# Optimization experiments

Hardware: AMD Instinct MI355X
Metric: run time of the kernel (lower is better)

Reference implementation:

```python
import jax, jax.numpy as jnp
import numpy as np


def setup_inputs() -> dict:
    key = jax.random.key(0)
    k1, k2, k3 = jax.random.split(key, 3)
    B, T, S, D = 8, 2048, 2048, 512
    main_input = jax.random.normal(k1, (B, T, D), dtype=jnp.float32)
    attn_input = jax.random.normal(k2, (B, S, D), dtype=jnp.float32)
    # f_input is a torch Linear(D, D): y = x @ W_f.T + b_f
    W_f = jax.random.normal(k3, (D, D), dtype=jnp.float32) * (1.0 / np.sqrt(D))
    b_f = jnp.zeros((D,), dtype=jnp.float32)
    return {"main_input": main_input, "attn_input": attn_input, "W_f": W_f, "b_f": b_f}


def reference(main_input, attn_input, W_f, b_f):
    # keys: f_input applied to each attn word  [B,S,D]
    keys = jnp.einsum("bsd,ed->bse", attn_input, W_f) + b_f
    # scores[b,t,s] = keys[b,s,:] . main_input[b,t,:]
    scores = jnp.einsum("bse,bte->bts", keys, main_input)
    attn = jax.nn.softmax(scores, axis=-1)  # softmax over attn words S
    # weighted sum of RAW attn_input (values are unprojected)
    out = jnp.einsum("bts,bsd->btd", attn, attn_input)
    return out
```

## Files before the change

### kernel.cpp

```cpp
#include <hip/hip_runtime.h>
#include <math.h>

#define B_  8
#define T_  2048
#define S_  2048
#define D_  512

typedef _Float16 half8   __attribute__((ext_vector_type(8)));
typedef _Float16 half4_t __attribute__((ext_vector_type(4)));
typedef float    floatx4 __attribute__((ext_vector_type(4)));

__device__ __forceinline__ floatx4 mfma16(half8 a, half8 b, floatx4 c) {
  return __builtin_amdgcn_mfma_f32_16x16x32_f16(a, b, c, 0, 0, 0);
}

__device__ __forceinline__ void async16(void* lds, const void* g) {
  __builtin_amdgcn_global_load_lds(
      (const __attribute__((address_space(1))) void*)g,
      (__attribute__((address_space(3))) void*)lds, 16, 0, 0);
}

__global__ __launch_bounds__(256) void transpose_cast_kernel(
    const float* __restrict__ attn, _Float16* __restrict__ Vt) {
  __shared__ _Float16 tile[32][33];
  const int tx = threadIdx.x, ty = threadIdx.y;
  const int b = blockIdx.z, s0 = blockIdx.y * 32, d0 = blockIdx.x * 32;
  const float* src = attn + ((size_t)b * S_ + s0) * D_ + d0;
#pragma unroll
  for (int i = 0; i < 4; ++i) {
    int s = ty + i * 8;
    tile[tx][s] = (_Float16)src[(size_t)s * D_ + tx];
  }
  __syncthreads();
  _Float16* dst = Vt + ((size_t)b * D_ + d0) * S_ + s0;
#pragma unroll
  for (int i = 0; i < 4; ++i) {
    int d = ty + i * 8;
    dst[(size_t)d * S_ + tx] = tile[d][tx];
  }
}

__global__ __launch_bounds__(512, 2) void keys_gemm_kernel(
    const float* __restrict__ X, const float* __restrict__ W,
    const float* __restrict__ bias, _Float16* __restrict__ K16) {
  __shared__ alignas(16) _Float16 Xs[128][72];
  __shared__ alignas(16) _Float16 Ws[128][72];
  const int t = threadIdx.x;
  const int wave = t >> 6, lane = t & 63, q = lane >> 4, n = lane & 15;
  const int wm = wave >> 2, wn = wave & 3;
  const int m0 = blockIdx.x * 128, n0 = blockIdx.y * 128;

  floatx4 acc[4][2];
#pragma unroll
  for (int i = 0; i < 4; ++i)
#pragma unroll
    for (int j = 0; j < 2; ++j) {
      floatx4 z = {0.f, 0.f, 0.f, 0.f};
      acc[i][j] = z;
    }

  for (int kc = 0; kc < 8; ++kc) {
    const int k0 = kc * 64;
#pragma unroll
    for (int i = 0; i < 4; ++i) {
      int seg = i * 512 + t;
      int row = seg >> 4, c4 = (seg & 15) * 4;
      floatx4 xv = *(const floatx4*)&X[(size_t)(m0 + row) * D_ + k0 + c4];
      floatx4 wv = *(const floatx4*)&W[(size_t)(n0 + row) * D_ + k0 + c4];
      half4_t xh, wh;
#pragma unroll
      for (int j = 0; j < 4; ++j) { xh[j] = (_Float16)xv[j]; wh[j] = (_Float16)wv[j]; }
      *(half4_t*)&Xs[row][c4] = xh;
      *(half4_t*)&Ws[row][c4] = wh;
    }
    __syncthreads();
#pragma unroll
    for (int kk = 0; kk < 2; ++kk) {
      half8 a[4], bb[2];
#pragma unroll
      for (int mt = 0; mt < 4; ++mt)
        a[mt] = *(const half8*)&Xs[wm * 64 + mt * 16 + n][kk * 32 + q * 8];
#pragma unroll
      for (int nt = 0; nt < 2; ++nt)
        bb[nt] = *(const half8*)&Ws[wn * 32 + nt * 16 + n][kk * 32 + q * 8];
#pragma unroll
      for (int mt = 0; mt < 4; ++mt)
#pragma unroll
        for (int nt = 0; nt < 2; ++nt)
          acc[mt][nt] = mfma16(a[mt], bb[nt], acc[mt][nt]);
    }
    __syncthreads();
  }

#pragma unroll
  for (int nt = 0; nt < 2; ++nt) {
    int col = n0 + wn * 32 + nt * 16 + n;
    float bv = bias[col];
#pragma unroll
    for (int mt = 0; mt < 4; ++mt)
#pragma unroll
      for (int r = 0; r < 4; ++r) {
        int row = m0 + wm * 64 + mt * 16 + q * 4 + r;
        K16[(size_t)row * D_ + col] = (_Float16)(acc[mt][nt][r] + bv);
      }
  }
}

__global__ __launch_bounds__(256, 1) void flash_kernel(
    const float* __restrict__ Qf, const _Float16* __restrict__ K16,
    const _Float16* __restrict__ Vt, float* __restrict__ out) {
  __shared__ _Float16 Klds[2][32][512];
  __shared__ _Float16 Vlds[2][512][32];
  __shared__ _Float16 Pscr[4][16][40];

  const int t = threadIdx.x;
  const int w = t >> 6, lane = t & 63, qd = lane >> 4, n = lane & 15;
  const int n7 = n & 7;
  const int bid = blockIdx.x;
  const int b = bid & 7, t0 = (bid >> 3) * 64;

  const _Float16* Kb = K16 + (size_t)b * S_ * D_;
  const _Float16* Vb = Vt + (size_t)b * D_ * S_;

  const int ksw = lane ^ 0;
  const int vsw = (lane & 3) ^ ((lane >> 3) & 3);
  const int ccV = qd ^ ((n >> 1) & 3);

  half8 qreg[16];
  {
    const float* qrow = Qf + ((size_t)b * T_ + t0 + w * 16 + n) * D_;
#pragma unroll
    for (int kk = 0; kk < 16; ++kk) {
      floatx4 v0 = *(const floatx4*)&qrow[kk * 32 + qd * 8];
      floatx4 v1 = *(const floatx4*)&qrow[kk * 32 + qd * 8 + 4];
      half8 h;
#pragma unroll
      for (int j = 0; j < 4; ++j) { h[j] = (_Float16)v0[j]; h[j + 4] = (_Float16)v1[j]; }
      qreg[kk] = h;
    }
  }

  floatx4 O[33];
#pragma unroll
  for (int ng = 0; ng < 33; ++ng) {
    floatx4 z = {0.f, 0.f, 0.f, 0.f};
    O[ng] = z;
  }
  float m_st[4];
#pragma unroll
  for (int r = 0; r < 4; ++r) m_st[r] = -1e30f;

  half8 ones8;
#pragma unroll
  for (int j = 0; j < 8; ++j) ones8[j] = (_Float16)1.0f;

#pragma unroll
  for (int i = 0; i < 8; ++i) {
    int row = w * 8 + i;
    async16(&Klds[0][row][0], Kb + (size_t)row * D_ + ((lane ^ (row & 7)) * 8));
  }
#pragma unroll
  for (int i = 0; i < 8; ++i) {
    int d0 = (w * 8 + i) * 16;
    async16(&Vlds[0][d0][0], Vb + (size_t)(d0 + (lane >> 2)) * S_ + vsw * 8);
  }
  __syncthreads();

  for (int st = 0; st < S_ / 32; ++st) {
    const int cur = st & 1, nxt = cur ^ 1;
    const int s0 = st * 32;

    if (st < S_ / 32 - 1) {
#pragma unroll
      for (int i = 0; i < 8; ++i) {
        int row = w * 8 + i;
        async16(&Klds[nxt][row][0],
                Kb + (size_t)(s0 + 32 + row) * D_ + ((lane ^ (row & 7)) * 8));
      }
#pragma unroll
      for (int i = 0; i < 8; ++i) {
        int d0 = (w * 8 + i) * 16;
        async16(&Vlds[nxt][d0][0],
                Vb + (size_t)(d0 + (lane >> 2)) * S_ + s0 + 32 + vsw * 8);
      }
    }

    floatx4 Sa0 = {0.f, 0.f, 0.f, 0.f}, Sa1 = Sa0, Sb0 = Sa0, Sb1 = Sa0;
#pragma unroll
    for (int kk = 0; kk < 8; ++kk) {
      int slot = (kk * 4 + qd) ^ n7;
      half8 b0 = *(const half8*)&Klds[cur][n][slot * 8];
      half8 b1 = *(const half8*)&Klds[cur][16 + n][slot * 8];
      Sa0 = mfma16(qreg[kk], b0, Sa0);
      Sa1 = mfma16(qreg[kk], b1, Sa1);
    }
#pragma unroll
    for (int kk = 8; kk < 16; ++kk) {
      int slot = (kk * 4 + qd) ^ n7;
      half8 b0 = *(const half8*)&Klds[cur][n][slot * 8];
      half8 b1 = *(const half8*)&Klds[cur][16 + n][slot * 8];
      Sb0 = mfma16(qreg[kk], b0, Sb0);
      Sb1 = mfma16(qreg[kk], b1, Sb1);
    }
    floatx4 Sc0 = Sa0 + Sb0, Sc1 = Sa1 + Sb1;

    float alpha[4];
#pragma unroll
    for (int r = 0; r < 4; ++r) {
      float v = fmaxf(Sc0[r], Sc1[r]);
      v = fmaxf(v, __shfl_xor(v, 1, 16));
      v = fmaxf(v, __shfl_xor(v, 2, 16));
      v = fmaxf(v, __shfl_xor(v, 4, 16));
      v = fmaxf(v, __shfl_xor(v, 8, 16));
      float mn = fmaxf(m_st[r], v);
      alpha[r] = __expf(m_st[r] - mn);
      m_st[r] = mn;
    }

    bool unchanged = (alpha[0] == 1.f) & (alpha[1] == 1.f) &
                     (alpha[2] == 1.f) & (alpha[3] == 1.f);
    if (!__all(unchanged)) {
#pragma unroll
      for (int ng = 0; ng < 33; ++ng)
#pragma unroll
        for (int r = 0; r < 4; ++r) O[ng][r] *= alpha[r];
    }

#pragma unroll
    for (int r = 0; r < 4; ++r) {
      float p0 = __expf(Sc0[r] - m_st[r]);
      float p1 = __expf(Sc1[r] - m_st[r]);
      Pscr[w][qd * 4 + r][n] = (_Float16)p0;
      Pscr[w][qd * 4 + r][16 + n] = (_Float16)p1;
    }
    half8 av = *(const half8*)&Pscr[w][n][qd * 8];

#pragma unroll
    for (int ng = 0; ng < 32; ++ng) {
      half8 bv = *(const half8*)&Vlds[cur][ng * 16 + n][ccV * 8];
      O[ng] = mfma16(av, bv, O[ng]);
    }
    O[32] = mfma16(av, ones8, O[32]);

    if (st < S_ / 32 - 1) __syncthreads();
  }

  float* ob = out + ((size_t)b * T_ + t0 + w * 16) * D_;
#pragma unroll
  for (int r = 0; r < 4; ++r) {
    float inv = 1.f / O[32][r];
    const size_t rowoff = (size_t)(qd * 4 + r) * D_;
#pragma unroll
    for (int ng = 0; ng < 32; ++ng)
      ob[rowoff + ng * 16 + n] = O[ng][r] * inv;
  }
}

extern "C" void kernel_launch(void* const* d_in, const int* in_sizes, int n_in,
                              void* d_out, int out_size, void* d_ws, size_t ws_size,
                              hipStream_t stream) {
  (void)in_sizes; (void)n_in; (void)out_size; (void)ws_size;
  const float* main_in = (const float*)d_in[0];
  const float* attn_in = (const float*)d_in[1];
  const float* W_f     = (const float*)d_in[2];
  const float* b_f     = (const float*)d_in[3];
  float* out = (float*)d_out;

  _Float16* K16 = (_Float16*)d_ws;
  _Float16* Vt  = K16 + (size_t)B_ * S_ * D_;

  transpose_cast_kernel<<<dim3(D_ / 32, S_ / 32, B_), dim3(32, 8, 1), 0, stream>>>(
      attn_in, Vt);
  keys_gemm_kernel<<<dim3((B_ * S_) / 128, D_ / 128), 512, 0, stream>>>(
      attn_in, W_f, b_f, K16);
  flash_kernel<<<(B_ * T_) / 64, 256, 0, stream>>>(main_in, K16, Vt, out);
}
```

Measured before the change: 314.2 us.

## Split flash output dim across 8 waves and prestage fp16 inputs for keys GEMM

The flash kernel now runs 8 waves per block. Two waves share each 16-row query group and each computes half of the 512-wide output, which halves the O accumulator registers and targets two blocks per CU. The Q·K score computation is now done twice, once by each of the two waves in a pair. The keys GEMM now reads fp16 copies of X (written by the transpose kernel) and W (written by a new cast kernel) through async global-to-LDS loads with double buffering and 4x4 MFMA tiles per wave. This adds an extra fp16 workspace write plus one more kernel launch, and the V LDS swizzle was removed, which may cause bank conflicts.

```diff
diff --git a/kernel.cpp b/kernel.cpp
--- a/kernel.cpp
+++ b/kernel.cpp
@@ -21,7 +21,8 @@
 }
 
 __global__ __launch_bounds__(256) void transpose_cast_kernel(
-    const float* __restrict__ attn, _Float16* __restrict__ Vt) {
+    const float* __restrict__ attn, _Float16* __restrict__ Vt,
+    _Float16* __restrict__ X16) {
   __shared__ _Float16 tile[32][33];
   const int tx = threadIdx.x, ty = threadIdx.y;
   const int b = blockIdx.z, s0 = blockIdx.y * 32, d0 = blockIdx.x * 32;
@@ -29,7 +30,9 @@
 #pragma unroll
   for (int i = 0; i < 4; ++i) {
     int s = ty + i * 8;
-    tile[tx][s] = (_Float16)src[(size_t)s * D_ + tx];
+    _Float16 h = (_Float16)src[(size_t)s * D_ + tx];
+    tile[tx][s] = h;
+    X16[((size_t)b * S_ + s0 + s) * D_ + d0 + tx] = h;
   }
   __syncthreads();
   _Float16* dst = Vt + ((size_t)b * D_ + d0) * S_ + s0;
@@ -40,95 +43,105 @@
   }
 }
 
-__global__ __launch_bounds__(512, 2) void keys_gemm_kernel(
-    const float* __restrict__ X, const float* __restrict__ W,
+__global__ __launch_bounds__(256) void wcast_kernel(
+    const float* __restrict__ W, _Float16* __restrict__ W16) {
+  int idx = (blockIdx.x * 256 + threadIdx.x) * 4;
+  floatx4 v = *(const floatx4*)&W[idx];
+  half4_t h;
+#pragma unroll
+  for (int j = 0; j < 4; ++j) h[j] = (_Float16)v[j];
+  *(half4_t*)&W16[idx] = h;
+}
+
+__global__ __launch_bounds__(256, 2) void keys_gemm_kernel(
+    const _Float16* __restrict__ X16, const _Float16* __restrict__ W16,
     const float* __restrict__ bias, _Float16* __restrict__ K16) {
-  __shared__ alignas(16) _Float16 Xs[128][72];
-  __shared__ alignas(16) _Float16 Ws[128][72];
+  __shared__ _Float16 As[2][128 * 32];
+  __shared__ _Float16 Bs[2][128 * 32];
   const int t = threadIdx.x;
-  const int wave = t >> 6, lane = t & 63, q = lane >> 4, n = lane & 15;
-  const int wm = wave >> 2, wn = wave & 3;
+  const int w = t >> 6, lane = t & 63, qd = lane >> 4, n = lane & 15;
+  const int wm = w >> 1, wn = w & 1;
   const int m0 = blockIdx.x * 128, n0 = blockIdx.y * 128;
 
-  floatx4 acc[4][2];
+  floatx4 acc[4][4];
 #pragma unroll
   for (int i = 0; i < 4; ++i)
 #pragma unroll
-    for (int j = 0; j < 2; ++j) {
+    for (int j = 0; j < 4; ++j) {
       floatx4 z = {0.f, 0.f, 0.f, 0.f};
       acc[i][j] = z;
     }
 
-  for (int kc = 0; kc < 8; ++kc) {
-    const int k0 = kc * 64;
-#pragma unroll
-    for (int i = 0; i < 4; ++i) {
-      int seg = i * 512 + t;
-      int row = seg >> 4, c4 = (seg & 15) * 4;
-      floatx4 xv = *(const floatx4*)&X[(size_t)(m0 + row) * D_ + k0 + c4];
-      floatx4 wv = *(const floatx4*)&W[(size_t)(n0 + row) * D_ + k0 + c4];
-      half4_t xh, wh;
-#pragma unroll
-      for (int j = 0; j < 4; ++j) { xh[j] = (_Float16)xv[j]; wh[j] = (_Float16)wv[j]; }
-      *(half4_t*)&Xs[row][c4] = xh;
-      *(half4_t*)&Ws[row][c4] = wh;
-    }
+  const int srow = (lane >> 2);
+  const int schunk = (lane & 3) * 8;
+
+  auto stage = [&](int buf, int k0) {
+#pragma unroll
+    for (int i = 0; i < 2; ++i) {
+      int row = w * 32 + i * 16;
+      async16(&As[buf][row * 32],
+              X16 + (size_t)(m0 + row + srow) * D_ + k0 + schunk);
+      async16(&Bs[buf][row * 32],
+              W16 + (size_t)(n0 + row + srow) * D_ + k0 + schunk);
+    }
+  };
+
+  stage(0, 0);
+  __syncthreads();
+
+  for (int ks = 0; ks < 16; ++ks) {
+    const int cur = ks & 1;
+    if (ks < 15) stage(cur ^ 1, (ks + 1) * 32);
+
+    half8 a[4], bb[4];
+#pragma unroll
+    for (int mt = 0; mt < 4; ++mt)
+      a[mt] = *(const half8*)&As[cur][(wm * 64 + mt * 16 + n) * 32 + qd * 8];
+#pragma unroll
+    for (int nt = 0; nt < 4; ++nt)
+      bb[nt] = *(const half8*)&Bs[cur][(wn * 64 + nt * 16 + n) * 32 + qd * 8];
+#pragma unroll
+    for (int mt = 0; mt < 4; ++mt)
+#pragma unroll
+      for (int nt = 0; nt < 4; ++nt)
+        acc[mt][nt] = mfma16(a[mt], bb[nt], acc[mt][nt]);
+
     __syncthreads();
-#pragma unroll
-    for (int kk = 0; kk < 2; ++kk) {
-      half8 a[4], bb[2];
-#pragma unroll
-      for (int mt = 0; mt < 4; ++mt)
-        a[mt] = *(const half8*)&Xs[wm * 64 + mt * 16 + n][kk * 32 + q * 8];
-#pragma unroll
-      for (int nt = 0; nt < 2; ++nt)
-        bb[nt] = *(const half8*)&Ws[wn * 32 + nt * 16 + n][kk * 32 + q * 8];
-#pragma unroll
-      for (int mt = 0; mt < 4; ++mt)
-#pragma unroll
-        for (int nt = 0; nt < 2; ++nt)
-          acc[mt][nt] = mfma16(a[mt], bb[nt], acc[mt][nt]);
-    }
-    __syncthreads();
-  }
-
-#pragma unroll
-  for (int nt = 0; nt < 2; ++nt) {
-    int col = n0 + wn * 32 + nt * 16 + n;
+  }
+
+#pragma unroll
+  for (int nt = 0; nt < 4; ++nt) {
+    int col = n0 + wn * 64 + nt * 16 + n;
     float bv = bias[col];
 #pragma unroll
     for (int mt = 0; mt < 4; ++mt)
 #pragma unroll
       for (int r = 0; r < 4; ++r) {
-        int row = m0 + wm * 64 + mt * 16 + q * 4 + r;
+        int row = m0 + wm * 64 + mt * 16 + qd * 4 + r;
         K16[(size_t)row * D_ + col] = (_Float16)(acc[mt][nt][r] + bv);
       }
   }
 }
 
-__global__ __launch_bounds__(256, 1) void flash_kernel(
+__global__ __launch_bounds__(512, 2) void flash_kernel(
     const float* __restrict__ Qf, const _Float16* __restrict__ K16,
     const _Float16* __restrict__ Vt, float* __restrict__ out) {
   __shared__ _Float16 Klds[2][32][512];
   __shared__ _Float16 Vlds[2][512][32];
-  __shared__ _Float16 Pscr[4][16][40];
+  __shared__ _Float16 Pscr[8][16][40];
 
   const int t = threadIdx.x;
   const int w = t >> 6, lane = t & 63, qd = lane >> 4, n = lane & 15;
-  const int n7 = n & 7;
+  const int rg = w & 3, dh = w >> 2;
   const int bid = blockIdx.x;
   const int b = bid & 7, t0 = (bid >> 3) * 64;
 
   const _Float16* Kb = K16 + (size_t)b * S_ * D_;
   const _Float16* Vb = Vt + (size_t)b * D_ * S_;
 
-  const int ksw = lane ^ 0;
-  const int vsw = (lane & 3) ^ ((lane >> 3) & 3);
-  const int ccV = qd ^ ((n >> 1) & 3);
-
   half8 qreg[16];
   {
-    const float* qrow = Qf + ((size_t)b * T_ + t0 + w * 16 + n) * D_;
+    const float* qrow = Qf + ((size_t)b * T_ + t0 + rg * 16 + n) * D_;
 #pragma unroll
     for (int kk = 0; kk < 16; ++kk) {
       floatx4 v0 = *(const floatx4*)&qrow[kk * 32 + qd * 8];
@@ -140,9 +153,9 @@
     }
   }
 
-  floatx4 O[33];
-#pragma unroll
-  for (int ng = 0; ng < 33; ++ng) {
+  floatx4 O[17];
+#pragma unroll
+  for (int ng = 0; ng < 17; ++ng) {
     floatx4 z = {0.f, 0.f, 0.f, 0.f};
     O[ng] = z;
   }
@@ -154,55 +167,47 @@
 #pragma unroll
   for (int j = 0; j < 8; ++j) ones8[j] = (_Float16)1.0f;
 
-#pragma unroll
-  for (int i = 0; i < 8; ++i) {
-    int row = w * 8 + i;
-    async16(&Klds[0][row][0], Kb + (size_t)row * D_ + ((lane ^ (row & 7)) * 8));
-  }
-#pragma unroll
-  for (int i = 0; i < 8; ++i) {
-    int d0 = (w * 8 + i) * 16;
-    async16(&Vlds[0][d0][0], Vb + (size_t)(d0 + (lane >> 2)) * S_ + vsw * 8);
-  }
+  auto stageK = [&](int buf, int s0) {
+#pragma unroll
+    for (int i = 0; i < 4; ++i) {
+      int srow = w * 4 + i;
+      async16(&Klds[buf][srow][0],
+              Kb + (size_t)(s0 + srow) * D_ + ((lane ^ (srow & 7)) * 8));
+    }
+  };
+  auto stageV = [&](int buf, int s0) {
+#pragma unroll
+    for (int i = 0; i < 4; ++i) {
+      int d0 = (w * 4 + i) * 16;
+      async16(&Vlds[buf][d0][0],
+              Vb + (size_t)(d0 + (lane >> 2)) * S_ + s0 + (lane & 3) * 8);
+    }
+  };
+
+  stageK(0, 0);
+  stageV(0, 0);
   __syncthreads();
 
+  const int n7 = n & 7;
+
   for (int st = 0; st < S_ / 32; ++st) {
-    const int cur = st & 1, nxt = cur ^ 1;
+    const int cur = st & 1;
     const int s0 = st * 32;
 
     if (st < S_ / 32 - 1) {
-#pragma unroll
-      for (int i = 0; i < 8; ++i) {
-        int row = w * 8 + i;
-        async16(&Klds[nxt][row][0],
-                Kb + (size_t)(s0 + 32 + row) * D_ + ((lane ^ (row & 7)) * 8));
-      }
-#pragma unroll
-      for (int i = 0; i < 8; ++i) {
-        int d0 = (w * 8 + i) * 16;
-        async16(&Vlds[nxt][d0][0],
-                Vb + (size_t)(d0 + (lane >> 2)) * S_ + s0 + 32 + vsw * 8);
-      }
-    }
-
-    floatx4 Sa0 = {0.f, 0.f, 0.f, 0.f}, Sa1 = Sa0, Sb0 = Sa0, Sb1 = Sa0;
-#pragma unroll
-    for (int kk = 0; kk < 8; ++kk) {
-      int slot = (kk * 4 + qd) ^ n7;
-      half8 b0 = *(const half8*)&Klds[cur][n][slot * 8];
-      half8 b1 = *(const half8*)&Klds[cur][16 + n][slot * 8];
-      Sa0 = mfma16(qreg[kk], b0, Sa0);
-      Sa1 = mfma16(qreg[kk], b1, Sa1);
-    }
-#pragma unroll
-    for (int kk = 8; kk < 16; ++kk) {
-      int slot = (kk * 4 + qd) ^ n7;
-      half8 b0 = *(const half8*)&Klds[cur][n][slot * 8];
-      half8 b1 = *(const half8*)&Klds[cur][16 + n][slot * 8];
-      Sb0 = mfma16(qreg[kk], b0, Sb0);
-      Sb1 = mfma16(qreg[kk], b1, Sb1);
-    }
-    floatx4 Sc0 = Sa0 + Sb0, Sc1 = Sa1 + Sb1;
+      stageK(cur ^ 1, s0 + 32);
+      stageV(cur ^ 1, s0 + 32);
+    }
+
+    floatx4 Sc0 = {0.f, 0.f, 0.f, 0.f}, Sc1 = Sc0;
+#pragma unroll
+    for (int kk = 0; kk < 16; ++kk) {
+      int slot = ((kk * 4 + qd) ^ n7) * 8;
+      half8 b0 = *(const half8*)&Klds[cur][n][slot];
+      half8 b1 = *(const half8*)&Klds[cur][16 + n][slot];
+      Sc0 = mfma16(qreg[kk], b0, Sc0);
+      Sc1 = mfma16(qreg[kk], b1, Sc1);
+    }
 
     float alpha[4];
 #pragma unroll
@@ -221,7 +226,7 @@
                      (alpha[2] == 1.f) & (alpha[3] == 1.f);
     if (!__all(unchanged)) {
 #pragma unroll
-      for (int ng = 0; ng < 33; ++ng)
+      for (int ng = 0; ng < 17; ++ng)
 #pragma unroll
         for (int r = 0; r < 4; ++r) O[ng][r] *= alpha[r];
     }
@@ -236,22 +241,22 @@
     half8 av = *(const half8*)&Pscr[w][n][qd * 8];
 
 #pragma unroll
-    for (int ng = 0; ng < 32; ++ng) {
-      half8 bv = *(const half8*)&Vlds[cur][ng * 16 + n][ccV * 8];
+    for (int ng = 0; ng < 16; ++ng) {
+      half8 bv = *(const half8*)&Vlds[cur][dh * 256 + ng * 16 + n][qd * 8];
       O[ng] = mfma16(av, bv, O[ng]);
     }
-    O[32] = mfma16(av, ones8, O[32]);
+    O[16] = mfma16(av, ones8, O[16]);
 
     if (st < S_ / 32 - 1) __syncthreads();
   }
 
-  float* ob = out + ((size_t)b * T_ + t0 + w * 16) * D_;
+  float* ob = out + ((size_t)b * T_ + t0 + rg * 16) * D_ + dh * 256;
 #pragma unroll
   for (int r = 0; r < 4; ++r) {
-    float inv = 1.f / O[32][r];
+    float inv = 1.f / O[16][r];
     const size_t rowoff = (size_t)(qd * 4 + r) * D_;
 #pragma unroll
-    for (int ng = 0; ng < 32; ++ng)
+    for (int ng = 0; ng < 16; ++ng)
       ob[rowoff + ng * 16 + n] = O[ng][r] * inv;
   }
 }
@@ -268,10 +273,13 @@
 
   _Float16* K16 = (_Float16*)d_ws;
   _Float16* Vt  = K16 + (size_t)B_ * S_ * D_;
+  _Float16* X16 = Vt + (size_t)B_ * D_ * S_;
+  _Float16* W16 = X16 + (size_t)B_ * S_ * D_;
 
   transpose_cast_kernel<<<dim3(D_ / 32, S_ / 32, B_), dim3(32, 8, 1), 0, stream>>>(
-      attn_in, Vt);
-  keys_gemm_kernel<<<dim3((B_ * S_) / 128, D_ / 128), 512, 0, stream>>>(
-      attn_in, W_f, b_f, K16);
-  flash_kernel<<<(B_ * T_) / 64, 256, 0, stream>>>(main_in, K16, Vt, out);
-}
+      attn_in, Vt, X16);
+  wcast_kernel<<<(D_ * D_) / (256 * 4), 256, 0, stream>>>(W_f, W16);
+  keys_gemm_kernel<<<dim3((B_ * S_) / 128, D_ / 128), 256, 0, stream>>>(
+      X16, W16, b_f, K16);
+  flash_kernel<<<(B_ * T_) / 64, 512, 0, stream>>>(main_in, K16, Vt, out);
+}
```

Result: no change. 316.4 us (+0.7%).
